# Kernel tuning notes

Measured on AMD Instinct MI355X. Metric: run time of the kernel, lower is better.

Reference implementation:

```python
import jax, jax.numpy as jnp
import numpy as np

D_OUT = 1024

def setup_inputs() -> dict:
    key = jax.random.key(0)
    k1, k2, k3, k4 = jax.random.split(key, 4)
    x = jax.random.normal(k1, (4, 2048, 1024), dtype=jnp.float32)
    # torch.nn.Linear weights are [d_out, d_in]
    s = 1.0 / np.sqrt(1024)
    W_q = jax.random.uniform(k2, (D_OUT, 1024), dtype=jnp.float32, minval=-s, maxval=s)
    W_k = jax.random.uniform(k3, (D_OUT, 1024), dtype=jnp.float32, minval=-s, maxval=s)
    W_v = jax.random.uniform(k4, (D_OUT, 1024), dtype=jnp.float32, minval=-s, maxval=s)
    return {"x": x, "W_q": W_q, "W_k": W_k, "W_v": W_v}

def reference(x, W_q, W_k, W_v):
    b, n, d_in = x.shape
    q = jnp.einsum('bnd,od->bno', x, W_q)  # [b, n, d_out]
    k = jnp.einsum('bnd,od->bno', x, W_k)
    v = jnp.einsum('bnd,od->bno', x, W_v)
    scores = jnp.einsum('bqd,bkd->bqk', q, k)  # full N x N score matrix
    causal = jnp.tril(jnp.ones((n, n), dtype=bool))
    scores = jnp.where(causal, scores, -jnp.inf)
    weights = jax.nn.softmax(scores / jnp.sqrt(jnp.float32(D_OUT)), axis=-1)
    # dropout p=0.0 -> identity (eval)
    return jnp.einsum('bqk,bkd->bqd', weights, v)
```

## Files before the change

kernel.cpp:

```cpp
#include <hip/hip_runtime.h>
#include <hip/hip_bf16.h>
#include <stdint.h>
#include <math.h>

typedef unsigned short ushort_t;
typedef __attribute__((ext_vector_type(4))) float f32x4;
typedef __attribute__((ext_vector_type(8))) __bf16 bf16x8;
typedef __attribute__((ext_vector_type(8))) unsigned short ushort8;
typedef __attribute__((ext_vector_type(4))) unsigned short ushort4v;

__device__ __forceinline__ float bf2f(ushort_t u) {
  union { unsigned u32; float f; } x; x.u32 = ((unsigned)u) << 16; return x.f;
}
__device__ __forceinline__ ushort_t f2bf(float f) {
  union { float f; unsigned u; } x; x.f = f;
  unsigned r = x.u + 0x7FFF + ((x.u >> 16) & 1);
  return (ushort_t)(r >> 16);
}

__device__ __forceinline__ void gld16(const ushort_t* g, ushort_t* l) {
  __builtin_amdgcn_global_load_lds(
      (const __attribute__((address_space(1))) uint32_t*)g,
      (__attribute__((address_space(3))) uint32_t*)l, 16, 0, 0);
}

__global__ __launch_bounds__(256) void cast_all_kernel(
    const float* __restrict__ x, const float* __restrict__ wq,
    const float* __restrict__ wk, const float* __restrict__ wv,
    ushort_t* __restrict__ xb, ushort_t* __restrict__ wqb,
    ushort_t* __restrict__ wkb, ushort_t* __restrict__ wvb,
    float* __restrict__ rowsum) {
  int blk = blockIdx.x;
  if (blk >= 4096 + 1536) {
    int idx = (blk - (4096 + 1536)) * 256 + threadIdx.x;
    f32x4 z = {0.f, 0.f, 0.f, 0.f};
    ((f32x4*)rowsum)[idx * 2] = z;
    ((f32x4*)rowsum)[idx * 2 + 1] = z;
    return;
  }
  const float* in;
  ushort_t* out;
  int i;
  if (blk < 4096) {
    in = x; out = xb; i = blk * 256 + threadIdx.x;
  } else {
    int w = (blk - 4096) >> 9;
    int lb = (blk - 4096) & 511;
    in = (w == 0) ? wq : (w == 1) ? wk : wv;
    out = (w == 0) ? wqb : (w == 1) ? wkb : wvb;
    i = lb * 256 + threadIdx.x;
  }
  const f32x4* p = (const f32x4*)in;
  f32x4 a = p[2 * i];
  f32x4 b = p[2 * i + 1];
  ushort8 o;
  o[0] = f2bf(a[0]); o[1] = f2bf(a[1]); o[2] = f2bf(a[2]); o[3] = f2bf(a[3]);
  o[4] = f2bf(b[0]); o[5] = f2bf(b[1]); o[6] = f2bf(b[2]); o[7] = f2bf(b[3]);
  *((ushort8*)out + i) = o;
}

#define BM 128
#define BN 128
#define BK 64

__device__ __forceinline__ void gemm_core(
    const ushort_t* __restrict__ A, const ushort_t* __restrict__ B, int Kd,
    int kEnd, int m0, int n0, ushort_t* As, ushort_t* Bs, f32x4 (&acc)[4][4]) {
  int tid = threadIdx.x;
  int lane = tid & 63;
  int wave = tid >> 6;
  int wr = (wave >> 1) * 64;
  int wc = (wave & 1) * 64;
  int ln15 = lane & 15;
  int kq = lane >> 4;

  int row = tid >> 3;
  int ksw = ((tid & 7) ^ (row & 7)) * 8;
  const ushort_t* aB = A + (size_t)(m0 + row) * Kd + ksw;
  const ushort_t* bB = B + (size_t)(n0 + row) * Kd + ksw;
  int xk = ln15 & 7;

  for (int k0 = 0; k0 < kEnd; k0 += BK) {
    __syncthreads();
#pragma unroll
    for (int r = 0; r < 4; ++r) {
      gld16(aB + (size_t)(32 * r) * Kd + k0, &As[(tid + 256 * r) * 8]);
      gld16(bB + (size_t)(32 * r) * Kd + k0, &Bs[(tid + 256 * r) * 8]);
    }
    __syncthreads();
#pragma unroll
    for (int s = 0; s < 2; ++s) {
      bf16x8 af[4], bfr[4];
#pragma unroll
      for (int i = 0; i < 4; ++i)
        af[i] = *(const bf16x8*)
            &As[(wr + i * 16 + ln15) * BK + (((s * 4 + kq) ^ xk) * 8)];
#pragma unroll
      for (int j = 0; j < 4; ++j)
        bfr[j] = *(const bf16x8*)
            &Bs[(wc + j * 16 + ln15) * BK + (((s * 4 + kq) ^ xk) * 8)];
#pragma unroll
      for (int i = 0; i < 4; ++i)
#pragma unroll
        for (int j = 0; j < 4; ++j)
          acc[i][j] = __builtin_amdgcn_mfma_f32_16x16x32_bf16(
              af[i], bfr[j], acc[i][j], 0, 0, 0);
    }
  }
}

__global__ __launch_bounds__(256, 3) void gemm_qk(
    const ushort_t* __restrict__ xb, const ushort_t* __restrict__ wq,
    const ushort_t* __restrict__ wk, ushort_t* __restrict__ Qb,
    ushort_t* __restrict__ Kb) {
  int m0 = blockIdx.x * BM, n0 = blockIdx.y * BN;
  int z = blockIdx.z;
  const ushort_t* B = (z == 0) ? wq : wk;

  __shared__ ushort_t As[BM * BK];
  __shared__ ushort_t Bs[BN * BK];

  f32x4 acc[4][4];
#pragma unroll
  for (int i = 0; i < 4; ++i)
#pragma unroll
    for (int j = 0; j < 4; ++j) acc[i][j] = f32x4{0.f, 0.f, 0.f, 0.f};

  gemm_core(xb, B, 1024, 1024, m0, n0, As, Bs, acc);

  int tid = threadIdx.x;
  int lane = tid & 63;
  int wave = tid >> 6;
  int wr = (wave >> 1) * 64;
  int wc = (wave & 1) * 64;
  int ln15 = lane & 15;
  int kq = lane >> 4;

  ushort_t* C = (z == 0) ? Qb : Kb;
#pragma unroll
  for (int i = 0; i < 4; ++i) {
    int row0 = m0 + wr + i * 16 + kq * 4;
#pragma unroll
    for (int j = 0; j < 4; ++j) {
      int col = n0 + wc + j * 16 + ln15;
#pragma unroll
      for (int r = 0; r < 4; ++r)
        C[(size_t)(row0 + r) * 1024 + col] = f2bf(acc[i][j][r]);
    }
  }
}

__global__ __launch_bounds__(256, 3) void gemm_sv(
    const ushort_t* __restrict__ Qg, const ushort_t* __restrict__ Kg,
    const ushort_t* __restrict__ xb, const ushort_t* __restrict__ wv,
    ushort_t* __restrict__ Eg, ushort_t* __restrict__ Vt,
    float scale, float* __restrict__ rowsum) {
  int L = blockIdx.x;
  int xcd = L & 7;
  int slot = L >> 3;
  int bz = xcd >> 1;
  int idx = ((xcd & 1) * 132) + slot;
  bool isS = idx < 136;
  int m0, n0;
  const ushort_t *A, *B;
  if (isS) {
    int t = idx;
    int m = (int)((sqrtf(8.f * (float)t + 1.f) - 1.f) * 0.5f);
    while ((m + 1) * (m + 2) / 2 <= t) ++m;
    while (m * (m + 1) / 2 > t) --m;
    int n = t - m * (m + 1) / 2;
    m0 = m * BM; n0 = n * BN;
    A = Qg + (size_t)bz * (2048 * 1024);
    B = Kg + (size_t)bz * (2048 * 1024);
  } else {
    int vid = (idx - 136) + 128 * bz;
    m0 = (vid >> 3) * BM;
    n0 = (vid & 7) * BN;
    A = xb;
    B = wv;
  }

  __shared__ ushort_t As[BM * BK];
  __shared__ ushort_t Bs[BN * BK];

  f32x4 acc[4][4];
#pragma unroll
  for (int i = 0; i < 4; ++i)
#pragma unroll
    for (int j = 0; j < 4; ++j) acc[i][j] = f32x4{0.f, 0.f, 0.f, 0.f};

  gemm_core(A, B, 1024, 1024, m0, n0, As, Bs, acc);

  int tid = threadIdx.x;
  int lane = tid & 63;
  int wave = tid >> 6;
  int wr = (wave >> 1) * 64;
  int wc = (wave & 1) * 64;
  int ln15 = lane & 15;
  int kq = lane >> 4;

  if (isS) {
    ushort_t* C = Eg + (size_t)bz * (2048 * 2048);
    float* rs = rowsum + (size_t)bz * 2048;
#pragma unroll
    for (int i = 0; i < 4; ++i) {
      int row0 = m0 + wr + i * 16 + kq * 4;
#pragma unroll
      for (int r = 0; r < 4; ++r) {
        int grow = row0 + r;
        float psum = 0.f;
#pragma unroll
        for (int j = 0; j < 4; ++j) {
          int col = n0 + wc + j * 16 + ln15;
          float e = (col <= grow) ? __expf(acc[i][j][r] * scale) : 0.f;
          C[(size_t)grow * 2048 + col] = f2bf(e);
          psum += e;
        }
        psum += __shfl_xor(psum, 1);
        psum += __shfl_xor(psum, 2);
        psum += __shfl_xor(psum, 4);
        psum += __shfl_xor(psum, 8);
        if (ln15 == 0) atomicAdd(&rs[grow], psum);
      }
    }
  } else {
#pragma unroll
    for (int i = 0; i < 4; ++i) {
      int gm = m0 + wr + i * 16 + kq * 4;
      int b = gm >> 11, nn = gm & 2047;
#pragma unroll
      for (int j = 0; j < 4; ++j) {
        int d = n0 + wc + j * 16 + ln15;
        ushort4v v;
#pragma unroll
        for (int r = 0; r < 4; ++r) v[r] = f2bf(acc[i][j][r]);
        *(ushort4v*)&Vt[(size_t)b * (2048 * 1024) + (size_t)d * 2048 + nn] = v;
      }
    }
  }
}

__global__ __launch_bounds__(256, 3) void gemm_o(
    const ushort_t* __restrict__ Eg, const ushort_t* __restrict__ Vg,
    float* __restrict__ Og, const float* __restrict__ rowsum) {
  int L = blockIdx.x;
  int xcd = L & 7;
  int slot = L >> 3;
  int bz = xcd >> 1;
  int idx = ((xcd & 1) * 64) + slot;
  int n = idx & 7;
  int mm = idx >> 3;
  int m = (mm & 1) ? (15 - (mm >> 1)) : (mm >> 1);
  int m0 = m * BM, n0 = n * BN;
  int kEnd = min(2048, m0 + BM);
  const ushort_t* A = Eg + (size_t)bz * (2048 * 2048);
  const ushort_t* B = Vg + (size_t)bz * (1024 * 2048);

  __shared__ ushort_t As[BM * BK];
  __shared__ ushort_t Bs[BN * BK];

  f32x4 acc[4][4];
#pragma unroll
  for (int i = 0; i < 4; ++i)
#pragma unroll
    for (int j = 0; j < 4; ++j) acc[i][j] = f32x4{0.f, 0.f, 0.f, 0.f};

  gemm_core(A, B, 2048, kEnd, m0, n0, As, Bs, acc);

  int tid = threadIdx.x;
  int lane = tid & 63;
  int wave = tid >> 6;
  int wr = (wave >> 1) * 64;
  int wc = (wave & 1) * 64;
  int ln15 = lane & 15;
  int kq = lane >> 4;

  float* C = Og + (size_t)bz * (2048 * 1024);
  const float* rs = rowsum + (size_t)bz * 2048;
#pragma unroll
  for (int i = 0; i < 4; ++i) {
    int row0 = m0 + wr + i * 16 + kq * 4;
#pragma unroll
    for (int r = 0; r < 4; ++r) {
      float inv = 1.0f / rs[row0 + r];
#pragma unroll
      for (int j = 0; j < 4; ++j) {
        int col = n0 + wc + j * 16 + ln15;
        C[(size_t)(row0 + r) * 1024 + col] = acc[i][j][r] * inv;
      }
    }
  }
}

extern "C" void kernel_launch(void* const* d_in, const int* in_sizes, int n_in,
                              void* d_out, int out_size, void* d_ws, size_t ws_size,
                              hipStream_t stream) {
  const float* x = (const float*)d_in[0];
  const float* Wq = (const float*)d_in[1];
  const float* Wk = (const float*)d_in[2];
  const float* Wv = (const float*)d_in[3];
  float* out = (float*)d_out;
  char* ws = (char*)d_ws;

  ushort_t* xb = (ushort_t*)(ws);
  ushort_t* wqb = (ushort_t*)(ws + (16ull << 20));
  ushort_t* wkb = (ushort_t*)(ws + (18ull << 20));
  ushort_t* wvb = (ushort_t*)(ws + (20ull << 20));
  ushort_t* Qb = (ushort_t*)(ws + (22ull << 20));
  ushort_t* Kb = (ushort_t*)(ws + (38ull << 20));
  ushort_t* Vt = (ushort_t*)(ws + (54ull << 20));
  ushort_t* Eb = (ushort_t*)(ws + (70ull << 20));
  float* rowsum = (float*)(ws + (102ull << 20));

  cast_all_kernel<<<4096 + 3 * 512 + 4, 256, 0, stream>>>(
      x, Wq, Wk, Wv, xb, wqb, wkb, wvb, rowsum);

  dim3 gQK(8192 / BM, 1024 / BN, 2);
  gemm_qk<<<gQK, 256, 0, stream>>>(xb, wqb, wkb, Qb, Kb);

  gemm_sv<<<dim3(1056, 1, 1), 256, 0, stream>>>(
      Qb, Kb, xb, wvb, Eb, Vt, 0.03125f, rowsum);

  gemm_o<<<dim3(512, 1, 1), 256, 0, stream>>>(Eb, Vt, out, rowsum);
}
```

Baseline: 209.0 us.

## Remap blocks across XCDs for L2 locality and stage V transpose through LDS

The QK projection launch is flattened to a 1D grid and remapped so that each XCD pair works on one batch's rows, with the two XCDs of a pair splitting rows by parity. This is meant to keep shared A and B tiles inside one XCD's L2. The score/V kernel now splits causal S tiles between the two XCDs of a pair by column parity, and the V tiles are reassigned to match. The V transpose is staged through a swizzled LDS buffer so that Vt is written with coalesced 16-byte stores instead of scattered 8-byte stores. The gemm_o row ordering is flipped between the two XCDs. Together these add index arithmetic and extra barriers.

```diff
diff --git a/kernel.cpp b/kernel.cpp
--- a/kernel.cpp
+++ b/kernel.cpp
@@ -113,9 +113,17 @@
     const ushort_t* __restrict__ xb, const ushort_t* __restrict__ wq,
     const ushort_t* __restrict__ wk, ushort_t* __restrict__ Qb,
     ushort_t* __restrict__ Kb) {
-  int m0 = blockIdx.x * BM, n0 = blockIdx.y * BN;
-  int z = blockIdx.z;
-  const ushort_t* B = (z == 0) ? wq : wk;
+  int L = blockIdx.x;
+  int xcd = L & 7;
+  int slot = L >> 3;
+  int bz = xcd >> 1, p = xcd & 1;
+  int zz = slot >> 6;
+  int tt = slot & 63;
+  int m_local = ((tt >> 3) << 1) + p;
+  int n = tt & 7;
+  int m0 = (bz * 16 + m_local) * BM;
+  int n0 = n * BN;
+  const ushort_t* B = (zz == 0) ? wq : wk;
 
   __shared__ ushort_t As[BM * BK];
   __shared__ ushort_t Bs[BN * BK];
@@ -136,7 +144,7 @@
   int ln15 = lane & 15;
   int kq = lane >> 4;
 
-  ushort_t* C = (z == 0) ? Qb : Kb;
+  ushort_t* C = (zz == 0) ? Qb : Kb;
 #pragma unroll
   for (int i = 0; i < 4; ++i) {
     int row0 = m0 + wr + i * 16 + kq * 4;
@@ -158,30 +166,33 @@
   int L = blockIdx.x;
   int xcd = L & 7;
   int slot = L >> 3;
-  int bz = xcd >> 1;
-  int idx = ((xcd & 1) * 132) + slot;
-  bool isS = idx < 136;
+  int bz = xcd >> 1, p = xcd & 1;
+  int nS = p ? 64 : 72;
+  bool isS = slot < nS;
   int m0, n0;
   const ushort_t *A, *B;
   if (isS) {
-    int t = idx;
-    int m = (int)((sqrtf(8.f * (float)t + 1.f) - 1.f) * 0.5f);
-    while ((m + 1) * (m + 2) / 2 <= t) ++m;
-    while (m * (m + 1) / 2 > t) --m;
-    int n = t - m * (m + 1) / 2;
+    int t = slot, m = 0;
+    for (;;) {
+      int c = p ? ((m + 1) >> 1) : ((m >> 1) + 1);
+      if (t < c) break;
+      t -= c; ++m;
+    }
+    int n = 2 * t + p;
     m0 = m * BM; n0 = n * BN;
     A = Qg + (size_t)bz * (2048 * 1024);
     B = Kg + (size_t)bz * (2048 * 1024);
   } else {
-    int vid = (idx - 136) + 128 * bz;
-    m0 = (vid >> 3) * BM;
-    n0 = (vid & 7) * BN;
+    int vsl = (slot - nS) + (p ? 60 : 0);
+    m0 = (bz * 16 + (vsl >> 3)) * BM;
+    n0 = (vsl & 7) * BN;
     A = xb;
     B = wv;
   }
 
-  __shared__ ushort_t As[BM * BK];
-  __shared__ ushort_t Bs[BN * BK];
+  __shared__ ushort_t Sh[2 * BM * BK];
+  ushort_t* As = Sh;
+  ushort_t* Bs = Sh + BM * BK;
 
   f32x4 acc[4][4];
 #pragma unroll
@@ -224,18 +235,32 @@
       }
     }
   } else {
+    __syncthreads();
+    ushort_t* T = Sh;
 #pragma unroll
     for (int i = 0; i < 4; ++i) {
-      int gm = m0 + wr + i * 16 + kq * 4;
-      int b = gm >> 11, nn = gm & 2047;
+      int row0 = wr + i * 16 + kq * 4;
 #pragma unroll
       for (int j = 0; j < 4; ++j) {
-        int d = n0 + wc + j * 16 + ln15;
+        int col = wc + j * 16 + ln15;
+        int swz = (col & 7) << 3;
         ushort4v v;
 #pragma unroll
         for (int r = 0; r < 4; ++r) v[r] = f2bf(acc[i][j][r]);
-        *(ushort4v*)&Vt[(size_t)b * (2048 * 1024) + (size_t)d * 2048 + nn] = v;
+        *(ushort4v*)&T[col * 128 + (row0 ^ swz)] = v;
       }
+    }
+    __syncthreads();
+    int b = m0 >> 11, nn = m0 & 2047;
+    int d_l = tid & 127;
+    int tok0 = (tid >> 7) * 64;
+    int swz = (d_l & 7) << 3;
+    ushort_t* dst = &Vt[(size_t)b * (2048 * 1024) + (size_t)(n0 + d_l) * 2048 +
+                        nn + tok0];
+#pragma unroll
+    for (int k = 0; k < 8; ++k) {
+      ushort8 v = *(const ushort8*)&T[d_l * 128 + ((tok0 + 8 * k) ^ swz)];
+      *(ushort8*)&dst[8 * k] = v;
     }
   }
 }
@@ -250,7 +275,7 @@
   int idx = ((xcd & 1) * 64) + slot;
   int n = idx & 7;
   int mm = idx >> 3;
-  int m = (mm & 1) ? (15 - (mm >> 1)) : (mm >> 1);
+  int m = (mm & 1) ? (mm >> 1) : (15 - (mm >> 1));
   int m0 = m * BM, n0 = n * BN;
   int kEnd = min(2048, m0 + BM);
   const ushort_t* A = Eg + (size_t)bz * (2048 * 2048);
@@ -315,8 +340,7 @@
   cast_all_kernel<<<4096 + 3 * 512 + 4, 256, 0, stream>>>(
       x, Wq, Wk, Wv, xb, wqb, wkb, wvb, rowsum);
 
-  dim3 gQK(8192 / BM, 1024 / BN, 2);
-  gemm_qk<<<gQK, 256, 0, stream>>>(xb, wqb, wkb, Qb, Kb);
+  gemm_qk<<<dim3(1024, 1, 1), 256, 0, stream>>>(xb, wqb, wkb, Qb, Kb);
 
   gemm_sv<<<dim3(1056, 1, 1), 256, 0, stream>>>(
       Qb, Kb, xb, wvb, Eb, Vt, 0.03125f, rowsum);
```

After: 211.0 us. Within noise of the previous version (+1.0%).
